# Optimization experiments

Hardware: AMD Instinct MI355X
Metric: run time of the kernel (lower is better)

## Reference

```python
import jax, jax.numpy as jnp
import numpy as np

T, B, E, H = 2048, 2, 1024, 16
Dh = E // H


def setup_inputs() -> dict:
    key = jax.random.key(0)
    ks = jax.random.split(key, 5)
    s = 0.02
    query = jax.random.normal(ks[0], (T, B, E), dtype=jnp.float32)
    Wq = jax.random.normal(ks[1], (E, E), dtype=jnp.float32) * s
    Wk = jax.random.normal(ks[2], (E, E), dtype=jnp.float32) * s
    Wv = jax.random.normal(ks[3], (E, E), dtype=jnp.float32) * s
    Wo = jax.random.normal(ks[4], (E, E), dtype=jnp.float32) * s
    bq = jnp.zeros((E,), jnp.float32)
    bk = jnp.zeros((E,), jnp.float32)
    bv = jnp.zeros((E,), jnp.float32)
    bo = jnp.zeros((E,), jnp.float32)
    # additive causal mask: 0 on/below diagonal, -inf above (standard fairseq usage)
    neg = jnp.finfo(jnp.float32).min
    attn_mask = jnp.where(jnp.triu(jnp.ones((T, T), jnp.bool_), k=1), neg, 0.0).astype(jnp.float32)
    return {"query": query, "Wq": Wq, "bq": bq, "Wk": Wk, "bk": bk,
            "Wv": Wv, "bv": bv, "Wo": Wo, "bo": bo, "attn_mask": attn_mask}


def reference(query, Wq, bq, Wk, bk, Wv, bv, Wo, bo, attn_mask):
    t, b, e = query.shape
    scale = Dh ** -0.5
    # self-attention projections (nn.Linear: x @ W.T + b)
    q = (query @ Wq.T + bq) * scale  # [T,B,E]
    k = query @ Wk.T + bk
    v = query @ Wv.T + bv
    # [T, B*H, Dh] -> [B*H, T, Dh]
    q = q.reshape(t, b * H, Dh).transpose(1, 0, 2)
    k = k.reshape(t, b * H, Dh).transpose(1, 0, 2)
    v = v.reshape(t, b * H, Dh).transpose(1, 0, 2)
    # explicit bmm -> softmax -> bmm (materializes [B*H, T, T])
    attn_weights = jnp.einsum('btd,bsd->bts', q, k) + attn_mask[None, :, :]
    attn_probs = jax.nn.softmax(attn_weights, axis=-1)
    attn = jnp.einsum('bts,bsd->btd', attn_probs, v)  # [B*H, T, Dh]
    attn = attn.transpose(1, 0, 2).reshape(t, b, e)  # [T,B,E]
    out = attn @ Wo.T + bo
    return out
```

## Files before the change

### kernel.cpp

```cpp
#include <hip/hip_runtime.h>


typedef __attribute__((ext_vector_type(8))) short   s16x8;
typedef __attribute__((ext_vector_type(4))) float   f32x4;
typedef __attribute__((ext_vector_type(2))) __fp16  f16x2;
typedef __attribute__((ext_vector_type(4))) __fp16  f16x4;

#define MFMA16(a, b, c) __builtin_amdgcn_mfma_f32_16x16x32_bf16((a), (b), (c), 0, 0, 0)
#define MFMApv(a, b, c) __builtin_amdgcn_mfma_f32_16x16x16f16((a), (b), (c), 0, 0, 0)

static __device__ __forceinline__ unsigned short f2bf(float f) {
    unsigned u = __float_as_uint(f);
    unsigned r = u + 0x7fffu + ((u >> 16) & 1u);
    return (unsigned short)(r >> 16);
}

static __device__ __forceinline__ void gl2lds16(const void* g, void* l) {
    __builtin_amdgcn_global_load_lds(
        (const __attribute__((address_space(1))) unsigned int*)g,
        (__attribute__((address_space(3))) unsigned int*)l, 16, 0, 0);
}

__global__ __launch_bounds__(256) void cvt_all(const float* __restrict__ query,
                                               const float* __restrict__ w0,
                                               const float* __restrict__ w1,
                                               const float* __restrict__ w2,
                                               const float* __restrict__ w3,
                                               unsigned short* __restrict__ Xb,
                                               unsigned short* __restrict__ Wcat) {
    const int bx = blockIdx.x;
    if (bx < 4096) {
        const int i = threadIdx.x;
        const float4 f = reinterpret_cast<const float4*>(query + (size_t)bx * 1024)[i];
        ushort4 u;
        u.x = f2bf(f.x); u.y = f2bf(f.y); u.z = f2bf(f.z); u.w = f2bf(f.w);
        const int mrow = (bx & 1) * 2048 + (bx >> 1);
        reinterpret_cast<ushort4*>(Xb + (size_t)mrow * 1024)[i] = u;
    } else {
        const int j   = bx - 4096;
        const int sel = j >> 10;
        const int i   = (j & 1023) * 256 + threadIdx.x;
        const float* src = (sel == 0) ? w0 : (sel == 1) ? w1 : (sel == 2) ? w2 : w3;
        const float4 f = reinterpret_cast<const float4*>(src)[i];
        ushort4 u;
        u.x = f2bf(f.x); u.y = f2bf(f.y); u.z = f2bf(f.z); u.w = f2bf(f.w);
        reinterpret_cast<ushort4*>(Wcat + (size_t)sel * 1048576)[i] = u;
    }
}

__global__ __launch_bounds__(256) void gemm_qkv(const unsigned short* __restrict__ A,
                                                const unsigned short* __restrict__ W,
                                                const float* __restrict__ b0,
                                                const float* __restrict__ b1,
                                                const float* __restrict__ b2,
                                                unsigned short* __restrict__ outQK,
                                                __fp16* __restrict__ outV) {
    __shared__ __align__(16) unsigned short smem[16384];
    unsigned short* Al = smem;
    unsigned short* Bl = smem + 8192;

    const int tid  = threadIdx.x;
    const int w    = tid >> 6;
    const int lane = tid & 63;
    const int quad = lane >> 4;
    const int c    = lane & 15;
    const int wm   = w >> 1;
    const int wn   = w & 1;

    const int id   = blockIdx.x;
    const int xcd  = id & 7;
    const int slot = id >> 3;
    const int m0 = (xcd * 4 + (slot & 3)) * 128;
    const int n0 = (slot >> 2) * 128;

    f32x4 acc[4][4];
    #pragma unroll
    for (int mi = 0; mi < 4; ++mi)
        #pragma unroll
        for (int ni = 0; ni < 4; ++ni) acc[mi][ni] = (f32x4){0.f, 0.f, 0.f, 0.f};

    const int srow = tid >> 3;
    const int g    = (tid & 7) ^ (srow & 7);
    const unsigned short* aG = A + (size_t)(m0 + srow) * 1024 + g * 8;
    const unsigned short* wG = W + (size_t)(n0 + srow) * 1024 + g * 8;
    const int loff = tid * 8;

    const int cs = (c & 7);

    for (int kk = 0; kk < 16; ++kk) {
        const int k0 = kk * 64;
        __syncthreads();
        #pragma unroll
        for (int i = 0; i < 4; ++i) {
            gl2lds16(aG + k0 + i * 32 * 1024, &Al[loff + i * 2048]);
            gl2lds16(wG + k0 + i * 32 * 1024, &Bl[loff + i * 2048]);
        }
        __syncthreads();

        s16x8 af[4][2], bf[4][2];
        #pragma unroll
        for (int mi = 0; mi < 4; ++mi) {
            const int row = (wm * 64 + mi * 16 + c) * 64;
            af[mi][0] = *reinterpret_cast<const s16x8*>(&Al[row + ((quad ^ cs) << 3)]);
            af[mi][1] = *reinterpret_cast<const s16x8*>(&Al[row + (((4 + quad) ^ cs) << 3)]);
        }
        #pragma unroll
        for (int ni = 0; ni < 4; ++ni) {
            const int row = (wn * 64 + ni * 16 + c) * 64;
            bf[ni][0] = *reinterpret_cast<const s16x8*>(&Bl[row + ((quad ^ cs) << 3)]);
            bf[ni][1] = *reinterpret_cast<const s16x8*>(&Bl[row + (((4 + quad) ^ cs) << 3)]);
        }
        #pragma unroll
        for (int mi = 0; mi < 4; ++mi)
            #pragma unroll
            for (int ni = 0; ni < 4; ++ni) {
                acc[mi][ni] = MFMA16(af[mi][0], bf[ni][0], acc[mi][ni]);
                acc[mi][ni] = MFMA16(af[mi][1], bf[ni][1], acc[mi][ni]);
            }
    }

    const int sel = n0 >> 10;
    if (sel < 2) {
        const float scale = (sel == 0) ? 0.18033688011112042f : 1.0f;
        const float* bias = (sel == 0) ? b0 : b1;
        #pragma unroll
        for (int ni = 0; ni < 4; ++ni) {
            const int n = n0 + wn * 64 + ni * 16 + c;
            const float bval = bias[n & 1023];
            #pragma unroll
            for (int mi = 0; mi < 4; ++mi)
                #pragma unroll
                for (int r = 0; r < 4; ++r) {
                    const int m = m0 + wm * 64 + mi * 16 + quad * 4 + r;
                    outQK[(size_t)m * 2048 + n] = f2bf((acc[mi][ni][r] + bval) * scale);
                }
        }
    } else {
        __syncthreads();
        #pragma unroll
        for (int ni = 0; ni < 4; ++ni) {
            const int n = wn * 64 + ni * 16 + c;
            const float bval = b2[(n0 - 2048) + n];
            #pragma unroll
            for (int mi = 0; mi < 4; ++mi) {
                const int m = wm * 64 + mi * 16 + quad * 4;
                const f16x2 lo = __builtin_amdgcn_cvt_pkrtz(acc[mi][ni][0] + bval,
                                                            acc[mi][ni][1] + bval);
                const f16x2 hi = __builtin_amdgcn_cvt_pkrtz(acc[mi][ni][2] + bval,
                                                            acc[mi][ni][3] + bval);
                uint2 st;
                st.x = __builtin_bit_cast(unsigned int, lo);
                st.y = __builtin_bit_cast(unsigned int, hi);
                const int phys = n * 128 + (((m >> 3) ^ (n & 15)) << 3) + (m & 7);
                *reinterpret_cast<uint2*>(&smem[phys]) = st;
            }
        }
        __syncthreads();
        const int n = tid >> 1;
        const int vcol = (n0 - 2048) + n;
        const int bb = m0 >> 11, tbase = m0 & 2047;
        __fp16* vdst = outV + ((size_t)((bb * 16 + (vcol >> 6)) * 64 + (vcol & 63))) * 2048 + tbase;
        #pragma unroll
        for (int j = 0; j < 8; ++j) {
            const int lc = (tid & 1) * 8 + j;
            const int phys = n * 128 + ((lc ^ (n & 15)) << 3);
            *reinterpret_cast<uint4*>(vdst + lc * 8) =
                *reinterpret_cast<const uint4*>(&smem[phys]);
        }
    }
}

__global__ __launch_bounds__(256) void gemm_out(const unsigned short* __restrict__ A,
                                                const unsigned short* __restrict__ W,
                                                const float* __restrict__ bias,
                                                float* __restrict__ outF) {
    __shared__ __align__(16) unsigned short Al[64 * 64];
    __shared__ __align__(16) unsigned short Bl[128 * 64];

    const int tid  = threadIdx.x;
    const int w    = tid >> 6;
    const int lane = tid & 63;
    const int quad = lane >> 4;
    const int c    = lane & 15;

    const int id   = blockIdx.x;
    const int xcd  = id & 7;
    const int slot = id >> 3;
    const int m0 = (xcd * 8 + (slot & 7)) * 64;
    const int n0 = (slot >> 3) * 128;

    f32x4 acc[8];
    #pragma unroll
    for (int ni = 0; ni < 8; ++ni) acc[ni] = (f32x4){0.f, 0.f, 0.f, 0.f};

    const int srow = tid >> 3;
    const int g    = (tid & 7) ^ (srow & 7);
    const unsigned short* aG = A + (size_t)(m0 + srow) * 1024 + g * 8;
    const unsigned short* wG = W + (size_t)(n0 + srow) * 1024 + g * 8;
    const int loff = tid * 8;

    const int cs = (c & 7);

    for (int kk = 0; kk < 16; ++kk) {
        const int k0 = kk * 64;
        __syncthreads();
        gl2lds16(aG + k0,             &Al[loff]);
        gl2lds16(aG + k0 + 32 * 1024, &Al[loff + 2048]);
        #pragma unroll
        for (int i = 0; i < 4; ++i)
            gl2lds16(wG + k0 + i * 32 * 1024, &Bl[loff + i * 2048]);
        __syncthreads();

        const int arow = (w * 16 + c) * 64;
        const s16x8 af0 = *reinterpret_cast<const s16x8*>(&Al[arow + ((quad ^ cs) << 3)]);
        const s16x8 af1 = *reinterpret_cast<const s16x8*>(&Al[arow + (((4 + quad) ^ cs) << 3)]);
        #pragma unroll
        for (int ni = 0; ni < 8; ++ni) {
            const int brow = (ni * 16 + c) * 64;
            const s16x8 bf0 = *reinterpret_cast<const s16x8*>(&Bl[brow + ((quad ^ cs) << 3)]);
            const s16x8 bf1 = *reinterpret_cast<const s16x8*>(&Bl[brow + (((4 + quad) ^ cs) << 3)]);
            acc[ni] = MFMA16(af0, bf0, acc[ni]);
            acc[ni] = MFMA16(af1, bf1, acc[ni]);
        }
    }

    #pragma unroll
    for (int ni = 0; ni < 8; ++ni) {
        const int n = n0 + ni * 16 + c;
        const float bval = bias[n];
        const int m = m0 + w * 16 + quad * 4;
        const int bb = m >> 11, t = m & 2047;
        #pragma unroll
        for (int r = 0; r < 4; ++r)
            outF[(size_t)(2 * (t + r) + bb) * 1024 + n] = acc[ni][r] + bval;
    }
}

__global__ __launch_bounds__(256, 4) void attn_kernel(const unsigned short* __restrict__ QKb,
                                                      const __fp16* __restrict__ Vt,
                                                      unsigned short* __restrict__ Ob) {
    __shared__ unsigned short Kl[2][2][64][32];
    __shared__ __fp16 Vl[2][64][64];

    const int tid  = threadIdx.x;
    const int w    = tid >> 6;
    const int lane = tid & 63;
    const int quad = lane >> 4;
    const int c    = lane & 15;

    const int id = blockIdx.x;
    const int bh = (id & 7) * 4 + ((id >> 3) & 3);
    const int a  = 31 - (id >> 5);
    const int bB = bh >> 4, h = bh & 15;
    const int t0 = a * 64;
    const int trg = t0 + w * 16;
    const int nIt = a + 1;

    const unsigned short* qp = QKb + (size_t)(bB * 2048 + trg + c) * 2048 + h * 64 + quad * 8;
    const s16x8 aq0 = *reinterpret_cast<const s16x8*>(qp);
    const s16x8 aq1 = *reinterpret_cast<const s16x8*>(qp + 32);

    const int lr4 = lane >> 2, sl4 = lane & 3;
    const unsigned short* kSrc = QKb + (size_t)(bB * 2048 + w * 16 + lr4) * 2048
                                 + 1024 + h * 64 + (sl4 ^ ((lane >> 3) & 3)) * 8;
    const int vr8 = lane >> 3, sl8 = lane & 7;
    const __fp16* vSrcA = Vt + (size_t)(bh * 64 + w * 16 + vr8) * 2048 + (sl8 ^ vr8) * 8;
    const __fp16* vSrcB = vSrcA + (size_t)8 * 2048;

    f32x4 acc[4];
    float l = 0.f;
    #pragma unroll
    for (int dt = 0; dt < 4; ++dt) acc[dt] = (f32x4){0.f, 0.f, 0.f, 0.f};

    const int kswz = (quad ^ ((c >> 1) & 3)) * 8;

    {
        gl2lds16(kSrc,      &Kl[0][0][w * 16 + lr4][sl4 * 8]);
        gl2lds16(kSrc + 32, &Kl[0][1][w * 16 + lr4][sl4 * 8]);
        gl2lds16(vSrcA,     &Vl[0][w * 16 + vr8][sl8 * 8]);
        gl2lds16(vSrcB,     &Vl[0][w * 16 + 8 + vr8][sl8 * 8]);
    }

    for (int it = 0; it < nIt; ++it) {
        const int buf = it & 1;
        __syncthreads();
        if (it + 1 < nIt) {
            const size_t s1 = (size_t)(it + 1) * 64;
            const int nb = buf ^ 1;
            gl2lds16(kSrc + s1 * 2048,      &Kl[nb][0][w * 16 + lr4][sl4 * 8]);
            gl2lds16(kSrc + s1 * 2048 + 32, &Kl[nb][1][w * 16 + lr4][sl4 * 8]);
            gl2lds16(vSrcA + s1,            &Vl[nb][w * 16 + vr8][sl8 * 8]);
            gl2lds16(vSrcB + s1,            &Vl[nb][w * 16 + 8 + vr8][sl8 * 8]);
        }

        s16x8 kf[4][2];
        #pragma unroll
        for (int ns = 0; ns < 4; ++ns) {
            kf[ns][0] = *reinterpret_cast<const s16x8*>(&Kl[buf][0][ns * 16 + c][kswz]);
            kf[ns][1] = *reinterpret_cast<const s16x8*>(&Kl[buf][1][ns * 16 + c][kswz]);
        }
        f16x4 vf[4][4];
        #pragma unroll
        for (int dt = 0; dt < 4; ++dt)
            #pragma unroll
            for (int ch = 0; ch < 4; ++ch) {
                const int phys = ((2 * ch + (quad >> 1)) ^ (c & 7)) * 8 + (quad & 1) * 4;
                vf[dt][ch] = *reinterpret_cast<const f16x4*>(&Vl[buf][dt * 16 + c][phys]);
            }

        const int s0 = it * 64;
        const bool diag = (it == a);
        f32x4 sT[4];
        #pragma unroll
        for (int ns = 0; ns < 4; ++ns) {
            f32x4 z = (f32x4){0.f, 0.f, 0.f, 0.f};
            z = MFMA16(kf[ns][0], aq0, z);
            sT[ns] = MFMA16(kf[ns][1], aq1, z);
        }
        f16x4 pf[4];
        float lp = 0.f;
        #pragma unroll
        for (int ns = 0; ns < 4; ++ns) {
            float pv[4];
            #pragma unroll
            for (int r = 0; r < 4; ++r) pv[r] = exp2f(sT[ns][r]);
            if (diag) {
                const int sb = s0 + ns * 16 + quad * 4;
                const int qg = trg + c;
                #pragma unroll
                for (int r = 0; r < 4; ++r) if (sb + r > qg) pv[r] = 0.f;
            }
            lp += (pv[0] + pv[1]) + (pv[2] + pv[3]);
            const f16x2 lo = __builtin_amdgcn_cvt_pkrtz(pv[0], pv[1]);
            const f16x2 hi = __builtin_amdgcn_cvt_pkrtz(pv[2], pv[3]);
            pf[ns] = __builtin_shufflevector(lo, hi, 0, 1, 2, 3);
        }
        l += lp;
        #pragma unroll
        for (int dt = 0; dt < 4; ++dt)
            #pragma unroll
            for (int ns = 0; ns < 4; ++ns)
                acc[dt] = MFMApv(vf[dt][ns], pf[ns], acc[dt]);
    }

    float lv = l;
    lv += __shfl_xor(lv, 16);
    lv += __shfl_xor(lv, 32);
    const float inv = 1.0f / lv;
    const size_t base = (size_t)(bB * 2048 + trg + c) * 1024 + h * 64;
    #pragma unroll
    for (int dt = 0; dt < 4; ++dt) {
        const unsigned u0 = (unsigned)f2bf(acc[dt][0] * inv)
                          | ((unsigned)f2bf(acc[dt][1] * inv) << 16);
        const unsigned u1 = (unsigned)f2bf(acc[dt][2] * inv)
                          | ((unsigned)f2bf(acc[dt][3] * inv) << 16);
        uint2 st; st.x = u0; st.y = u1;
        *reinterpret_cast<uint2*>(Ob + base + dt * 16 + quad * 4) = st;
    }
}

extern "C" void kernel_launch(void* const* d_in, const int* in_sizes, int n_in,
                              void* d_out, int out_size, void* d_ws, size_t ws_size,
                              hipStream_t stream) {
    const float* query = (const float*)d_in[0];
    const float* Wq    = (const float*)d_in[1];
    const float* bq    = (const float*)d_in[2];
    const float* Wk    = (const float*)d_in[3];
    const float* bk    = (const float*)d_in[4];
    const float* Wv    = (const float*)d_in[5];
    const float* bv    = (const float*)d_in[6];
    const float* Wo    = (const float*)d_in[7];
    const float* bo    = (const float*)d_in[8];

    float* out = (float*)d_out;

    unsigned short* ws    = (unsigned short*)d_ws;
    unsigned short* Xbf   = ws;
    unsigned short* Wcat  = Xbf  + (size_t)4096 * 1024;
    unsigned short* QKb   = Wcat + (size_t)4 * 1024 * 1024;
    __fp16*         Vtw   = (__fp16*)(QKb + (size_t)4096 * 2048);
    unsigned short* attnb = (unsigned short*)(Vtw + (size_t)32 * 64 * 2048);

    cvt_all<<<8192, 256, 0, stream>>>(query, Wq, Wk, Wv, Wo, Xbf, Wcat);

    gemm_qkv<<<768, 256, 0, stream>>>(Xbf, Wcat, bq, bk, bv, QKb, Vtw);

    attn_kernel<<<1024, 256, 0, stream>>>(QKb, Vtw, attnb);

    gemm_out<<<512, 256, 0, stream>>>(attnb, Wcat + (size_t)3 * 1024 * 1024,
                                      bo, out);
}
```

Before: 199.7 us.

## Prefetch next K-tile into registers during MFMA in both projection GEMMs

```diff
diff --git a/kernel.cpp b/kernel.cpp
--- a/kernel.cpp
+++ b/kernel.cpp
@@ -87,15 +87,28 @@
 
     const int cs = (c & 7);
 
+    uint4 ra[4], rb[4];
+    #pragma unroll
+    for (int i = 0; i < 4; ++i) {
+        ra[i] = *reinterpret_cast<const uint4*>(aG + i * 32 * 1024);
+        rb[i] = *reinterpret_cast<const uint4*>(wG + i * 32 * 1024);
+    }
+    #pragma unroll
+    for (int i = 0; i < 4; ++i) {
+        *reinterpret_cast<uint4*>(&Al[loff + i * 2048]) = ra[i];
+        *reinterpret_cast<uint4*>(&Bl[loff + i * 2048]) = rb[i];
+    }
+    __syncthreads();
+
     for (int kk = 0; kk < 16; ++kk) {
-        const int k0 = kk * 64;
-        __syncthreads();
-        #pragma unroll
-        for (int i = 0; i < 4; ++i) {
-            gl2lds16(aG + k0 + i * 32 * 1024, &Al[loff + i * 2048]);
-            gl2lds16(wG + k0 + i * 32 * 1024, &Bl[loff + i * 2048]);
-        }
-        __syncthreads();
+        if (kk + 1 < 16) {
+            const int k1 = (kk + 1) * 64;
+            #pragma unroll
+            for (int i = 0; i < 4; ++i) {
+                ra[i] = *reinterpret_cast<const uint4*>(aG + k1 + i * 32 * 1024);
+                rb[i] = *reinterpret_cast<const uint4*>(wG + k1 + i * 32 * 1024);
+            }
+        }
 
         s16x8 af[4][2], bf[4][2];
         #pragma unroll
@@ -117,6 +130,16 @@
                 acc[mi][ni] = MFMA16(af[mi][0], bf[ni][0], acc[mi][ni]);
                 acc[mi][ni] = MFMA16(af[mi][1], bf[ni][1], acc[mi][ni]);
             }
+
+        __syncthreads();
+        if (kk + 1 < 16) {
+            #pragma unroll
+            for (int i = 0; i < 4; ++i) {
+                *reinterpret_cast<uint4*>(&Al[loff + i * 2048]) = ra[i];
+                *reinterpret_cast<uint4*>(&Bl[loff + i * 2048]) = rb[i];
+            }
+        }
+        __syncthreads();
     }
 
     const int sel = n0 >> 10;
@@ -136,7 +159,6 @@
                 }
         }
     } else {
-        __syncthreads();
         #pragma unroll
         for (int ni = 0; ni < 4; ++ni) {
             const int n = wn * 64 + ni * 16 + c;
@@ -201,15 +223,31 @@
 
     const int cs = (c & 7);
 
+    uint4 ra[2], rb[4];
+    #pragma unroll
+    for (int i = 0; i < 2; ++i)
+        ra[i] = *reinterpret_cast<const uint4*>(aG + i * 32 * 1024);
+    #pragma unroll
+    for (int i = 0; i < 4; ++i)
+        rb[i] = *reinterpret_cast<const uint4*>(wG + i * 32 * 1024);
+    #pragma unroll
+    for (int i = 0; i < 2; ++i)
+        *reinterpret_cast<uint4*>(&Al[loff + i * 2048]) = ra[i];
+    #pragma unroll
+    for (int i = 0; i < 4; ++i)
+        *reinterpret_cast<uint4*>(&Bl[loff + i * 2048]) = rb[i];
+    __syncthreads();
+
     for (int kk = 0; kk < 16; ++kk) {
-        const int k0 = kk * 64;
-        __syncthreads();
-        gl2lds16(aG + k0,             &Al[loff]);
-        gl2lds16(aG + k0 + 32 * 1024, &Al[loff + 2048]);
-        #pragma unroll
-        for (int i = 0; i < 4; ++i)
-            gl2lds16(wG + k0 + i * 32 * 1024, &Bl[loff + i * 2048]);
-        __syncthreads();
+        if (kk + 1 < 16) {
+            const int k1 = (kk + 1) * 64;
+            #pragma unroll
+            for (int i = 0; i < 2; ++i)
+                ra[i] = *reinterpret_cast<const uint4*>(aG + k1 + i * 32 * 1024);
+            #pragma unroll
+            for (int i = 0; i < 4; ++i)
+                rb[i] = *reinterpret_cast<const uint4*>(wG + k1 + i * 32 * 1024);
+        }
 
         const int arow = (w * 16 + c) * 64;
         const s16x8 af0 = *reinterpret_cast<const s16x8*>(&Al[arow + ((quad ^ cs) << 3)]);
@@ -222,6 +260,17 @@
             acc[ni] = MFMA16(af0, bf0, acc[ni]);
             acc[ni] = MFMA16(af1, bf1, acc[ni]);
         }
+
+        __syncthreads();
+        if (kk + 1 < 16) {
+            #pragma unroll
+            for (int i = 0; i < 2; ++i)
+                *reinterpret_cast<uint4*>(&Al[loff + i * 2048]) = ra[i];
+            #pragma unroll
+            for (int i = 0; i < 4; ++i)
+                *reinterpret_cast<uint4*>(&Bl[loff + i * 2048]) = rb[i];
+        }
+        __syncthreads();
     }
 
     #pragma unroll
```

After: 317.5 us. 59.0% more time.
